# Kernel tuning notes

Hardware: AMD Instinct MI355X
Metric: run time of the kernel (lower is better)

The kernel has to match this reference:

```python
import jax, jax.numpy as jnp
import numpy as np

BS, EMB, RES = 256, 768, 14
N_MASKS, HID, OUT, N_PROJ = 16, 4096, 256, 4
BN_EPS = 1e-5


def setup_inputs() -> dict:
    key = jax.random.key(0)
    ks = jax.random.split(key, 8)
    x = jax.random.normal(ks[0], (BS, EMB, RES, RES), jnp.float32)
    # binary ROI masks over the 14x14 = 196 patch grid
    masks = (jax.random.uniform(ks[1], (BS, N_MASKS, RES * RES)) < 0.3).astype(jnp.float32)
    projection_idx = jax.random.randint(ks[2], (N_MASKS,), 0, N_PROJ, jnp.int32)
    mask_ids = jax.random.randint(ks[3], (BS, N_MASKS), 0, 100, jnp.int32)
    # stacked params for the N_PROJ MLP projectors
    W1 = jax.random.normal(ks[4], (N_PROJ, EMB, HID), jnp.float32) * 0.02
    b1 = jnp.zeros((N_PROJ, HID), jnp.float32)
    gamma = jnp.ones((N_PROJ, HID), jnp.float32)
    beta = jnp.zeros((N_PROJ, HID), jnp.float32)
    W2 = jax.random.normal(ks[5], (N_PROJ, HID, OUT), jnp.float32) * 0.02
    b2 = jnp.zeros((N_PROJ, OUT), jnp.float32)
    return {"x": x, "masks": masks, "projection_idx": projection_idx,
            "mask_ids": mask_ids, "W1": W1, "b1": b1, "gamma": gamma,
            "beta": beta, "W2": W2, "b2": b2}


def reference(x, masks, projection_idx, mask_ids, W1, b1, gamma, beta, W2, b2):
    bs, emb, hx, hy = x.shape
    # [bs, emb, hx, hy] -> [bs, hw, emb]
    emb_local = jnp.transpose(x, (0, 2, 3, 1)).reshape(bs, hx * hy, emb)
    # mask-normalized pooling:  pooled[b,n,:] = mean of embeddings inside mask n
    area = masks.sum(axis=-1, keepdims=True)
    smpl = masks / jnp.maximum(area, 1.0)
    pooled = smpl @ emb_local                       # [bs, n_masks, emb]
    # dense dispatch: run EVERY projector over all pooled tokens (as original)
    h = jnp.einsum('bne,peh->pbnh', pooled, W1) + b1[:, None, None, :]
    # BatchNorm1d in training mode over flattened (bs*n_masks) batch, per projector
    mu = h.mean(axis=(1, 2), keepdims=True)
    var = jnp.mean(jnp.square(h - mu), axis=(1, 2), keepdims=True)  # biased var
    h = (h - mu) * jax.lax.rsqrt(var + BN_EPS) * gamma[:, None, None, :] + beta[:, None, None, :]
    h = jax.nn.relu(h)
    o = jnp.einsum('pbnh,pho->pbno', h, W2) + b2[:, None, None, :]   # [P, bs, n, out]
    # keep only projector projection_idx[n] for mask-slot n (disjoint selection)
    n_proj = W1.shape[0]
    sel = (projection_idx[None, :] == jnp.arange(n_proj)[:, None]).astype(o.dtype)  # [P, n]
    xs = (o * sel[:, None, :, None]).sum(axis=0)     # [bs, n_masks, out]
    return (xs, mask_ids)
```

## Files before the change

### kernel.cpp

```cpp
#include <hip/hip_runtime.h>
#include <hip/hip_bf16.h>

#define BS 256
#define EMB 768
#define HW 196
#define NMASK 16
#define HID 4096
#define OUT 256
#define NPROJ 4
#define MROWS 4096

typedef __attribute__((ext_vector_type(8))) short bf16x8;
typedef __attribute__((ext_vector_type(4))) float f32x4;
typedef __attribute__((ext_vector_type(8))) unsigned short u16x8;

__device__ inline float bf2f(unsigned short u) {
    unsigned int x = ((unsigned int)u) << 16;
    return __builtin_bit_cast(float, x);
}
__device__ inline short f2bfs(float f) {
    return __builtin_bit_cast(short, __float2bfloat16(f));
}

#define GL16(gptr, lptr)                                                     \
    __builtin_amdgcn_global_load_lds(                                        \
        (const __attribute__((address_space(1))) void*)(gptr),               \
        (__attribute__((address_space(3))) void*)(lptr), 16, 0, 0)

__global__ __launch_bounds__(256) void pool_mfma(
    const float* __restrict__ x, const float* __restrict__ masks,
    __hip_bfloat16* __restrict__ pooledG)
{
    __shared__ __align__(16) short afr[7 * 64 * 8];
    __shared__ float inv[NMASK];
    const int ec = blockIdx.x, b = blockIdx.y, tid = threadIdx.x;
    const float* mb = masks + (size_t)b * NMASK * HW;

    for (int s = tid; s < 7 * 64; s += 256) {
        int m = s & 15, kb = ((s >> 4) & 3) * 8 + (s >> 6) * 32;
        short v[8];
        #pragma unroll
        for (int j = 0; j < 8; ++j) {
            int kk = kb + j;
            v[j] = (kk < HW) ? f2bfs(mb[m * HW + kk]) : (short)0;
        }
        #pragma unroll
        for (int j = 0; j < 8; ++j) afr[s * 8 + j] = v[j];
    }
    if (tid >= 192) {
        int l = tid - 192, m = l >> 2, q = l & 3;
        float a = 0.f;
        for (int hw = q; hw < HW; hw += 4) a += mb[m * HW + hw];
        a += __shfl_xor(a, 1);
        a += __shfl_xor(a, 2);
        if (q == 0) inv[m] = 1.0f / fmaxf(a, 1.0f);
    }
    __syncthreads();

    const int lane = tid & 63, w = tid >> 6;
    const int lc = lane & 15, l4 = lane >> 4;
    const int ebase = ec * 192 + w * 48;
    const bf16x8* afv = (const bf16x8*)afr;
    f32x4 acc[3] = {};

    const float* xb0 = x + ((size_t)b * EMB + ebase + lc) * HW;

    for (int kc = 0; kc < 6; ++kc) {
        bf16x8 af = afv[kc * 64 + lane];
        float4 u[3][2];
        #pragma unroll
        for (int t = 0; t < 3; ++t) {
            const float* xr = xb0 + (size_t)(t * 16) * HW + kc * 32 + l4 * 8;
            u[t][0] = *(const float4*)(xr);
            u[t][1] = *(const float4*)(xr + 4);
        }
        #pragma unroll
        for (int t = 0; t < 3; ++t) {
            bf16x8 bf;
            bf[0] = f2bfs(u[t][0].x); bf[1] = f2bfs(u[t][0].y);
            bf[2] = f2bfs(u[t][0].z); bf[3] = f2bfs(u[t][0].w);
            bf[4] = f2bfs(u[t][1].x); bf[5] = f2bfs(u[t][1].y);
            bf[6] = f2bfs(u[t][1].z); bf[7] = f2bfs(u[t][1].w);
            acc[t] = __builtin_amdgcn_mfma_f32_16x16x32_bf16(af, bf, acc[t], 0, 0, 0);
        }
    }
    {
        bf16x8 af = afv[6 * 64 + lane];
        #pragma unroll
        for (int t = 0; t < 3; ++t) {
            bf16x8 bf = {};
            if (l4 == 0) {
                float4 u0 = *(const float4*)(xb0 + (size_t)(t * 16) * HW + 192);
                bf[0] = f2bfs(u0.x); bf[1] = f2bfs(u0.y);
                bf[2] = f2bfs(u0.z); bf[3] = f2bfs(u0.w);
            }
            acc[t] = __builtin_amdgcn_mfma_f32_16x16x32_bf16(af, bf, acc[t], 0, 0, 0);
        }
    }

    #pragma unroll
    for (int t = 0; t < 3; ++t) {
        int e = ebase + t * 16 + lc;
        #pragma unroll
        for (int j = 0; j < 4; ++j) {
            int m = l4 * 4 + j;
            pooledG[((size_t)m * 256 + b) * EMB + e] =
                __float2bfloat16(acc[t][j] * inv[m]);
        }
    }
}

__global__ __launch_bounds__(256) void prep(
    const float* __restrict__ W1, const float* __restrict__ W2,
    const __hip_bfloat16* __restrict__ pg,
    __hip_bfloat16* __restrict__ W1T, __hip_bfloat16* __restrict__ W2T,
    __hip_bfloat16* __restrict__ pgT)
{
    __shared__ __align__(16) char sm[64 * 65 * 4];
    const int bid = blockIdx.x, tid = threadIdx.x;
    if (bid < 4096) {
        const float* src; __hip_bfloat16* dst; int R, C, x, y, z;
        if (bid < 3072) { z = bid / 768; int r = bid % 768; x = r % 64; y = r / 64;
                          src = W1; dst = W1T; R = EMB; C = HID; }
        else            { int b2 = bid - 3072; z = b2 / 256; int r = b2 % 256;
                          x = r % 4; y = r / 4; src = W2; dst = W2T; R = HID; C = OUT; }
        float (*tile)[65] = (float(*)[65])sm;
        const float* s = src + (size_t)z * R * C;
        __hip_bfloat16* d = dst + (size_t)z * R * C;
        const int c0 = x * 64, r0 = y * 64;
        for (int i = tid; i < 4096; i += 256) {
            int r = i >> 6, c = i & 63;
            tile[r][c] = s[(size_t)(r0 + r) * C + c0 + c];
        }
        __syncthreads();
        for (int i = tid; i < 4096; i += 256) {
            int c = i >> 6, r = i & 63;
            d[(size_t)(c0 + c) * R + r0 + r] = __float2bfloat16(tile[r][c]);
        }
    } else {
        const int b3 = bid - 4096;
        const int x = b3 % 12, y = b3 / 12;
        __hip_bfloat16 (*tile)[65] = (__hip_bfloat16(*)[65])sm;
        const int c0 = x * 64, r0 = y * 64;
        for (int i = tid; i < 4096; i += 256) {
            int r = i >> 6, c = i & 63;
            tile[r][c] = pg[(size_t)(r0 + r) * EMB + c0 + c];
        }
        __syncthreads();
        for (int i = tid; i < 4096; i += 256) {
            int c = i >> 6, r = i & 63;
            pgT[(size_t)(c0 + c) * MROWS + r0 + r] = tile[r][c];
        }
    }
}

__global__ __launch_bounds__(256) void meanpool(
    const __hip_bfloat16* __restrict__ PT, float* __restrict__ mp)
{
    const int e = blockIdx.x, tid = threadIdx.x;
    const u16x8* p = (const u16x8*)(PT + (size_t)e * MROWS);
    u16x8 v1 = p[tid], v2 = p[tid + 256];
    float s = 0.f;
    #pragma unroll
    for (int j = 0; j < 8; ++j) s += bf2f((unsigned short)v1[j]) + bf2f((unsigned short)v2[j]);
    #pragma unroll
    for (int o = 1; o < 64; o <<= 1) s += __shfl_xor(s, o);
    __shared__ float wsum[4];
    if ((tid & 63) == 0) wsum[tid >> 6] = s;
    __syncthreads();
    if (tid == 0) mp[e] = (wsum[0] + wsum[1] + wsum[2] + wsum[3]) * (1.0f / 4096.0f);
}

__global__ __launch_bounds__(256) void cgemm(
    const __hip_bfloat16* __restrict__ PT, float* __restrict__ Cpart)
{
    __shared__ __align__(16) __hip_bfloat16 As[128 * 32];
    __shared__ __align__(16) __hip_bfloat16 Bs[128 * 32];
    const int tid = threadIdx.x, lane = tid & 63, wid = tid >> 6;
    const int n0 = blockIdx.x * 128, m0 = blockIdx.y * 128, kbase = blockIdx.z * 512;
    float* Cp = Cpart + (size_t)blockIdx.z * EMB * EMB;
    const int wr = wid >> 1, wc = wid & 1;
    const int l4 = lane >> 4, lc = lane & 15;

    f32x4 acc[4][4] = {};
    for (int k0 = kbase; k0 < kbase + 512; k0 += 32) {
        __syncthreads();
        #pragma unroll
        for (int r = 0; r < 2; ++r) {
            int t = r * 256 + tid;
            int row = t >> 2, ko = (t & 3) * 8;
            GL16(PT + (size_t)(m0 + row) * MROWS + k0 + ko, &As[(r * 256 + wid * 64) * 8]);
        }
        #pragma unroll
        for (int r = 0; r < 2; ++r) {
            int t = r * 256 + tid;
            int row = t >> 2, ko = (t & 3) * 8;
            GL16(PT + (size_t)(n0 + row) * MROWS + k0 + ko, &Bs[(r * 256 + wid * 64) * 8]);
        }
        __syncthreads();
        const bf16x8* Av = (const bf16x8*)As;
        const bf16x8* Bv = (const bf16x8*)Bs;
        bf16x8 a[4], b[4];
        #pragma unroll
        for (int m = 0; m < 4; ++m) a[m] = Av[(wr * 64 + m * 16 + lc) * 4 + l4];
        #pragma unroll
        for (int n = 0; n < 4; ++n) b[n] = Bv[(wc * 64 + n * 16 + lc) * 4 + l4];
        #pragma unroll
        for (int m = 0; m < 4; ++m)
            #pragma unroll
            for (int n = 0; n < 4; ++n)
                acc[m][n] = __builtin_amdgcn_mfma_f32_16x16x32_bf16(a[m], b[n], acc[m][n], 0, 0, 0);
    }
    #pragma unroll
    for (int m = 0; m < 4; ++m)
        #pragma unroll
        for (int n = 0; n < 4; ++n)
            #pragma unroll
            for (int j = 0; j < 4; ++j) {
                int row = m0 + wr * 64 + m * 16 + l4 * 4 + j;
                int col = n0 + wc * 64 + n * 16 + lc;
                Cp[(size_t)row * EMB + col] = acc[m][n][j];
            }
}

__global__ __launch_bounds__(256) void cvt_c(
    const float* __restrict__ Cpart, __hip_bfloat16* __restrict__ Cbf)
{
    int i = (blockIdx.x * 256 + threadIdx.x) * 4;
    float sx = 0.f, sy = 0.f, sz = 0.f, sw = 0.f;
    #pragma unroll
    for (int kz = 0; kz < 8; ++kz) {
        float4 v = *(const float4*)(Cpart + (size_t)kz * EMB * EMB + i);
        sx += v.x; sy += v.y; sz += v.z; sw += v.w;
    }
    const float s = 1.0f / 4096.0f;
    Cbf[i + 0] = __float2bfloat16(sx * s);
    Cbf[i + 1] = __float2bfloat16(sy * s);
    Cbf[i + 2] = __float2bfloat16(sz * s);
    Cbf[i + 3] = __float2bfloat16(sw * s);
}

__global__ __launch_bounds__(256) void ugemm(
    const __hip_bfloat16* __restrict__ W1T, const __hip_bfloat16* __restrict__ Cbf,
    const float* __restrict__ mp,
    float* __restrict__ Eh2p, float* __restrict__ Mup)
{
    __shared__ __align__(16) __hip_bfloat16 As[128 * 32];
    __shared__ __align__(16) __hip_bfloat16 Bs[128 * 32];
    const int tid = threadIdx.x, lane = tid & 63, wid = tid >> 6;
    const int n0 = blockIdx.x * 128, m0 = blockIdx.y * 128, p = blockIdx.z;
    const __hip_bfloat16* Ap = W1T + (size_t)p * HID * EMB;
    const int wr = wid >> 1, wc = wid & 1;
    const int l4 = lane >> 4, lc = lane & 15;

    f32x4 acc[4][4] = {};
    for (int k0 = 0; k0 < EMB; k0 += 32) {
        __syncthreads();
        #pragma unroll
        for (int r = 0; r < 2; ++r) {
            int t = r * 256 + tid;
            int row = t >> 2, ko = (t & 3) * 8;
            GL16(Ap + (size_t)(m0 + row) * EMB + k0 + ko, &As[(r * 256 + wid * 64) * 8]);
        }
        #pragma unroll
        for (int r = 0; r < 2; ++r) {
            int t = r * 256 + tid;
            int row = t >> 2, ko = (t & 3) * 8;
            GL16(Cbf + (size_t)(n0 + row) * EMB + k0 + ko, &Bs[(r * 256 + wid * 64) * 8]);
        }
        __syncthreads();
        const bf16x8* Av = (const bf16x8*)As;
        const bf16x8* Bv = (const bf16x8*)Bs;
        bf16x8 a[4], b[4];
        #pragma unroll
        for (int m = 0; m < 4; ++m) a[m] = Av[(wr * 64 + m * 16 + lc) * 4 + l4];
        #pragma unroll
        for (int n = 0; n < 4; ++n) b[n] = Bv[(wc * 64 + n * 16 + lc) * 4 + l4];
        #pragma unroll
        for (int m = 0; m < 4; ++m)
            #pragma unroll
            for (int n = 0; n < 4; ++n)
                acc[m][n] = __builtin_amdgcn_mfma_f32_16x16x32_bf16(a[m], b[n], acc[m][n], 0, 0, 0);
    }

    float mpv[4];
    #pragma unroll
    for (int n = 0; n < 4; ++n) mpv[n] = mp[n0 + wc * 64 + n * 16 + lc];
    #pragma unroll
    for (int m = 0; m < 4; ++m) {
        #pragma unroll
        for (int j = 0; j < 4; ++j) {
            int row = m0 + wr * 64 + m * 16 + l4 * 4 + j;
            const __hip_bfloat16* wrow = Ap + (size_t)row * EMB;
            float e2 = 0.f, mu = 0.f;
            #pragma unroll
            for (int n = 0; n < 4; ++n) {
                int col = n0 + wc * 64 + n * 16 + lc;
                float wv = bf2f(__builtin_bit_cast(unsigned short, wrow[col]));
                e2 += acc[m][n][j] * wv;
                mu += mpv[n] * wv;
            }
            e2 += __shfl_xor(e2, 1); e2 += __shfl_xor(e2, 2);
            e2 += __shfl_xor(e2, 4); e2 += __shfl_xor(e2, 8);
            mu += __shfl_xor(mu, 1); mu += __shfl_xor(mu, 2);
            mu += __shfl_xor(mu, 4); mu += __shfl_xor(mu, 8);
            if (lc == 0) {
                size_t idx = (((size_t)blockIdx.x * 2 + wc) * NPROJ + p) * HID + row;
                Eh2p[idx] = e2;
                Mup [idx] = mu;
            }
        }
    }
}

__global__ __launch_bounds__(256) void finalize(
    const float* __restrict__ Eh2p, const float* __restrict__ Mup,
    const float* __restrict__ gamma, const float* __restrict__ beta,
    float* __restrict__ sbuf, float* __restrict__ tbuf)
{
    int i = blockIdx.x * 256 + threadIdx.x;
    float e2 = 0.f, mu = 0.f;
    #pragma unroll
    for (int bx = 0; bx < 12; ++bx) {
        e2 += Eh2p[bx * (NPROJ * HID) + i];
        mu += Mup [bx * (NPROJ * HID) + i];
    }
    float var = e2 - mu * mu;
    float is  = rsqrtf(fmaxf(var, 0.0f) + 1e-5f);
    float sc  = gamma[i] * is;
    sbuf[i] = sc;
    tbuf[i] = beta[i] - mu * sc;
}

__global__ __launch_bounds__(512, 2) void gemm1_sel(
    const __hip_bfloat16* __restrict__ A, const __hip_bfloat16* __restrict__ W1T,
    const int* __restrict__ proj,
    const float* __restrict__ sbuf, const float* __restrict__ tbuf,
    __hip_bfloat16* __restrict__ hrelu)
{
    __shared__ __align__(16) short LS[3 * 16384];
    const int tid = threadIdx.x, lane = tid & 63, w = tid >> 6;
    const int wr = w >> 2, wc = w & 3;
    const int lc = lane & 15, l4 = lane >> 4;
    const int n0 = blockIdx.x * 256, m0 = blockIdx.y * 256;
    const int p = proj[blockIdx.y];
    const __hip_bfloat16* Ag = A;
    const __hip_bfloat16* Bg = W1T + (size_t)p * HID * EMB;
    const bf16x8* LSv = (const bf16x8*)LS;

    auto STAGE = [&](int t) {
        const int sb = (t % 3) * 32768;
        #pragma unroll
        for (int ab = 0; ab < 2; ++ab) {
            const __hip_bfloat16* g = ab ? Bg : Ag;
            const int rbase = ab ? n0 : m0;
            #pragma unroll
            for (int i = 0; i < 2; ++i) {
                int c = (w * 2 + i) * 64 + lane;
                int row = c >> 2, ps = c & 3;
                int ls = ps ^ (row & 3);
                const __hip_bfloat16* src =
                    g + (size_t)(rbase + row) * EMB + t * 32 + ls * 8;
                GL16(src, (char*)LS + sb + ab * 16384 + (w * 2 + i) * 1024);
            }
        }
    };

    f32x4 acc[8][4] = {};

    STAGE(0);
    STAGE(1);
    asm volatile("s_waitcnt vmcnt(4)" ::: "memory");
    __builtin_amdgcn_s_barrier();

    for (int t = 0; t < 24; ++t) {
        if (t + 2 < 24) STAGE(t + 2);
        const int vb = (t % 3) * 2048;

        bf16x8 bfr[4];
        #pragma unroll
        for (int nf = 0; nf < 4; ++nf) {
            int rb = wc * 64 + nf * 16 + lc;
            bfr[nf] = LSv[vb + 1024 + rb * 4 + (l4 ^ (rb & 3))];
        }
        #pragma unroll
        for (int q = 0; q < 4; ++q) {
            bf16x8 afr[2];
            #pragma unroll
            for (int m2 = 0; m2 < 2; ++m2) {
                int ra = wr * 128 + (q * 2 + m2) * 16 + lc;
                afr[m2] = LSv[vb + ra * 4 + (l4 ^ (ra & 3))];
            }
            __builtin_amdgcn_s_setprio(1);
            #pragma unroll
            for (int m2 = 0; m2 < 2; ++m2)
                #pragma unroll
                for (int nf = 0; nf < 4; ++nf)
                    acc[q * 2 + m2][nf] = __builtin_amdgcn_mfma_f32_16x16x32_bf16(
                        afr[m2], bfr[nf], acc[q * 2 + m2][nf], 0, 0, 0);
            __builtin_amdgcn_s_setprio(0);
        }

        if (t + 2 < 24) {
            asm volatile("s_waitcnt vmcnt(4)" ::: "memory");
            __builtin_amdgcn_s_barrier();
        } else if (t + 2 == 24) {
            asm volatile("s_waitcnt vmcnt(0)" ::: "memory");
            __builtin_amdgcn_s_barrier();
        }
    }

    #pragma unroll
    for (int nf = 0; nf < 4; ++nf) {
        int col = n0 + wc * 64 + nf * 16 + lc;
        float s = sbuf[p * HID + col];
        float tt = tbuf[p * HID + col];
        #pragma unroll
        for (int mf = 0; mf < 8; ++mf)
            #pragma unroll
            for (int j = 0; j < 4; ++j) {
                int row = m0 + wr * 128 + mf * 16 + l4 * 4 + j;
                float v = fmaxf(acc[mf][nf][j] * s + tt, 0.0f);
                hrelu[(size_t)row * HID + col] = __float2bfloat16(v);
            }
    }
}

__global__ __launch_bounds__(256) void gemm2(
    const __hip_bfloat16* __restrict__ Hn, const __hip_bfloat16* __restrict__ W2T,
    const int* __restrict__ proj, float* __restrict__ Opart)
{
    __shared__ __align__(16) __hip_bfloat16 As[128 * 32];
    __shared__ __align__(16) __hip_bfloat16 Bs[128 * 32];
    const int tid = threadIdx.x, lane = tid & 63, wid = tid >> 6;
    const int nmask = blockIdx.x;
    const int bc    = blockIdx.y;
    const int ct    = blockIdx.z >> 2, kz = blockIdx.z & 3;
    const int p = proj[nmask];
    const __hip_bfloat16* Ap = Hn + (size_t)(nmask * 256 + bc * 128) * HID;
    const __hip_bfloat16* Bp = W2T + ((size_t)p * OUT + ct * 128) * HID;
    float* Op = Opart + (size_t)kz * MROWS * OUT;
    const int wr = wid >> 1, wc = wid & 1;
    const int l4 = lane >> 4, lc = lane & 15;

    f32x4 acc[4][4] = {};
    for (int k0 = kz * 1024; k0 < kz * 1024 + 1024; k0 += 32) {
        __syncthreads();
        #pragma unroll
        for (int r = 0; r < 2; ++r) {
            int t = r * 256 + tid;
            int row = t >> 2, ko = (t & 3) * 8;
            GL16(Ap + (size_t)row * HID + k0 + ko, &As[(r * 256 + wid * 64) * 8]);
        }
        #pragma unroll
        for (int r = 0; r < 2; ++r) {
            int t = r * 256 + tid;
            int row = t >> 2, ko = (t & 3) * 8;
            GL16(Bp + (size_t)row * HID + k0 + ko, &Bs[(r * 256 + wid * 64) * 8]);
        }
        __syncthreads();
        const bf16x8* Av = (const bf16x8*)As;
        const bf16x8* Bv = (const bf16x8*)Bs;
        bf16x8 a[4], b[4];
        #pragma unroll
        for (int m = 0; m < 4; ++m) a[m] = Av[(wr * 64 + m * 16 + lc) * 4 + l4];
        #pragma unroll
        for (int n = 0; n < 4; ++n) b[n] = Bv[(wc * 64 + n * 16 + lc) * 4 + l4];
        #pragma unroll
        for (int m = 0; m < 4; ++m)
            #pragma unroll
            for (int n = 0; n < 4; ++n)
                acc[m][n] = __builtin_amdgcn_mfma_f32_16x16x32_bf16(a[m], b[n], acc[m][n], 0, 0, 0);
    }

    #pragma unroll
    for (int m = 0; m < 4; ++m)
        #pragma unroll
        for (int n = 0; n < 4; ++n)
            #pragma unroll
            for (int j = 0; j < 4; ++j) {
                int bb = bc * 128 + wr * 64 + m * 16 + l4 * 4 + j;
                int oc = ct * 128 + wc * 64 + n * 16 + lc;
                Op[((size_t)bb * NMASK + nmask) * OUT + oc] = acc[m][n][j];
            }
}

__global__ __launch_bounds__(256) void reduce_out(
    const float* __restrict__ Opart, const float* __restrict__ b2,
    const int* __restrict__ proj, const int* __restrict__ mids,
    float* __restrict__ out)
{
    int i = (blockIdx.x * 256 + threadIdx.x) * 4;
    float sx = 0.f, sy = 0.f, sz = 0.f, sw = 0.f;
    #pragma unroll
    for (int kz = 0; kz < 4; ++kz) {
        float4 v = *(const float4*)(Opart + (size_t)kz * MROWS * OUT + i);
        sx += v.x; sy += v.y; sz += v.z; sw += v.w;
    }
    int nm = (i >> 8) & 15;
    int p  = proj[nm];
    float4 bv = *(const float4*)(b2 + p * OUT + (i & 255));
    float4 r;
    r.x = sx + bv.x; r.y = sy + bv.y; r.z = sz + bv.z; r.w = sw + bv.w;
    *(float4*)(out + i) = r;
    if (blockIdx.x < 16) {
        int t = blockIdx.x * 256 + threadIdx.x;
        out[(size_t)MROWS * OUT + t] = (float)mids[t];
    }
}

extern "C" void kernel_launch(void* const* d_in, const int* in_sizes, int n_in,
                              void* d_out, int out_size, void* d_ws, size_t ws_size,
                              hipStream_t stream)
{
    const float* x     = (const float*)d_in[0];
    const float* masks = (const float*)d_in[1];
    const int*   proj  = (const int*)d_in[2];
    const int*   mids  = (const int*)d_in[3];
    const float* W1    = (const float*)d_in[4];
    const float* gamma = (const float*)d_in[6];
    const float* beta  = (const float*)d_in[7];
    const float* W2    = (const float*)d_in[8];
    const float* b2    = (const float*)d_in[9];
    float* out = (float*)d_out;

    char* ws = (char*)d_ws;
    __hip_bfloat16* pooledG = (__hip_bfloat16*)(ws);
    __hip_bfloat16* W1T     = (__hip_bfloat16*)(ws + 6291456);
    __hip_bfloat16* W2T     = (__hip_bfloat16*)(ws + 31457280);
    float*          mp      = (float*)(ws + 39845888);
    float*          Eh2p    = (float*)(ws + 39848960);
    float*          Mup     = (float*)(ws + 40635392);
    float*          sbuf    = (float*)(ws + 41421824);
    float*          tbuf    = (float*)(ws + 41487360);
    char* R = ws + 41552896;
    __hip_bfloat16* pooledT = (__hip_bfloat16*)(R);
    float*          Cpart   = (float*)(R + 6291456);
    __hip_bfloat16* Cbf     = (__hip_bfloat16*)(R + 25165824);
    __hip_bfloat16* hrelu   = (__hip_bfloat16*)(R);
    float*          Opart   = (float*)(R + 33554432);

    pool_mfma<<<dim3(4, BS), 256, 0, stream>>>(x, masks, pooledG);
    prep<<<4864, 256, 0, stream>>>(W1, W2, pooledG, W1T, W2T, pooledT);
    meanpool<<<EMB, 256, 0, stream>>>(pooledT, mp);
    cgemm<<<dim3(6, 6, 8), 256, 0, stream>>>(pooledT, Cpart);
    cvt_c<<<(EMB * EMB) / 1024, 256, 0, stream>>>(Cpart, Cbf);
    ugemm<<<dim3(6, 32, 4), 256, 0, stream>>>(W1T, Cbf, mp, Eh2p, Mup);
    finalize<<<(NPROJ * HID) / 256, 256, 0, stream>>>(Eh2p, Mup, gamma, beta, sbuf, tbuf);
    gemm1_sel<<<dim3(HID / 256, MROWS / 256), 512, 0, stream>>>(pooledG, W1T, proj, sbuf, tbuf, hrelu);
    gemm2<<<dim3(NMASK, 2, 8), 256, 0, stream>>>(hrelu, W2T, proj, Opart);
    reduce_out<<<(MROWS * OUT) / 1024, 256, 0, stream>>>(Opart, b2, proj, mids, out);
}
```

Before: 202.5 us.

## Fuse pooling with weight prep, fold meanpool and BN finalize into neighbors

Merges the pooling kernel with the W1/W2 transpose-convert kernel into one launch, so the two independent jobs can overlap across blocks. The per-embedding mean is now computed as per-batch partial sums inside pooling and reduced in the cvt_c kernel, which replaces the separate meanpool pass over the transposed pooled tensor. The BN finalize kernel is removed and its scale/shift is recomputed per block inside gemm1_sel and kept in shared memory. This cuts the launch count from ten to eight, at the cost of redundant finalize work across row-blocks and a serial 256-step reduction per thread in cvt_c.

```diff
diff --git a/kernel.cpp b/kernel.cpp
--- a/kernel.cpp
+++ b/kernel.cpp
@@ -27,107 +27,109 @@
         (const __attribute__((address_space(1))) void*)(gptr),               \
         (__attribute__((address_space(3))) void*)(lptr), 16, 0, 0)
 
-__global__ __launch_bounds__(256) void pool_mfma(
+__global__ __launch_bounds__(256) void fused_k1(
     const float* __restrict__ x, const float* __restrict__ masks,
-    __hip_bfloat16* __restrict__ pooledG)
-{
-    __shared__ __align__(16) short afr[7 * 64 * 8];
-    __shared__ float inv[NMASK];
-    const int ec = blockIdx.x, b = blockIdx.y, tid = threadIdx.x;
-    const float* mb = masks + (size_t)b * NMASK * HW;
-
-    for (int s = tid; s < 7 * 64; s += 256) {
-        int m = s & 15, kb = ((s >> 4) & 3) * 8 + (s >> 6) * 32;
-        short v[8];
-        #pragma unroll
-        for (int j = 0; j < 8; ++j) {
-            int kk = kb + j;
-            v[j] = (kk < HW) ? f2bfs(mb[m * HW + kk]) : (short)0;
-        }
-        #pragma unroll
-        for (int j = 0; j < 8; ++j) afr[s * 8 + j] = v[j];
-    }
-    if (tid >= 192) {
-        int l = tid - 192, m = l >> 2, q = l & 3;
-        float a = 0.f;
-        for (int hw = q; hw < HW; hw += 4) a += mb[m * HW + hw];
-        a += __shfl_xor(a, 1);
-        a += __shfl_xor(a, 2);
-        if (q == 0) inv[m] = 1.0f / fmaxf(a, 1.0f);
-    }
-    __syncthreads();
-
-    const int lane = tid & 63, w = tid >> 6;
-    const int lc = lane & 15, l4 = lane >> 4;
-    const int ebase = ec * 192 + w * 48;
-    const bf16x8* afv = (const bf16x8*)afr;
-    f32x4 acc[3] = {};
-
-    const float* xb0 = x + ((size_t)b * EMB + ebase + lc) * HW;
-
-    for (int kc = 0; kc < 6; ++kc) {
-        bf16x8 af = afv[kc * 64 + lane];
-        float4 u[3][2];
+    const float* __restrict__ W1, const float* __restrict__ W2,
+    __hip_bfloat16* __restrict__ pooledG,
+    __hip_bfloat16* __restrict__ W1T, __hip_bfloat16* __restrict__ W2T,
+    float* __restrict__ mpB)
+{
+    __shared__ __align__(16) char smu[16704];
+    const int bid = blockIdx.x, tid = threadIdx.x;
+
+    if (bid < 1024) {
+        short* afr = (short*)smu;
+        float* inv = (float*)(smu + 14592);
+        const int ec = bid & 3, b = bid >> 2;
+        const float* mb = masks + (size_t)b * NMASK * HW;
+
+        for (int s = tid; s < 7 * 64; s += 256) {
+            int m = s & 15, kb = ((s >> 4) & 3) * 8 + (s >> 6) * 32;
+            short v[8];
+            #pragma unroll
+            for (int j = 0; j < 8; ++j) {
+                int kk = kb + j;
+                v[j] = (kk < HW) ? f2bfs(mb[m * HW + kk]) : (short)0;
+            }
+            #pragma unroll
+            for (int j = 0; j < 8; ++j) afr[s * 8 + j] = v[j];
+        }
+        if (tid >= 192) {
+            int l = tid - 192, m = l >> 2, q = l & 3;
+            float a = 0.f;
+            for (int hw = q; hw < HW; hw += 4) a += mb[m * HW + hw];
+            a += __shfl_xor(a, 1);
+            a += __shfl_xor(a, 2);
+            if (q == 0) inv[m] = 1.0f / fmaxf(a, 1.0f);
+        }
+        __syncthreads();
+
+        const int lane = tid & 63, w = tid >> 6;
+        const int lc = lane & 15, l4 = lane >> 4;
+        const int ebase = ec * 192 + w * 48;
+        const bf16x8* afv = (const bf16x8*)afr;
+        f32x4 acc[3] = {};
+
+        const float* xb0 = x + ((size_t)b * EMB + ebase + lc) * HW;
+
+        for (int kc = 0; kc < 6; ++kc) {
+            bf16x8 af = afv[kc * 64 + lane];
+            float4 u[3][2];
+            #pragma unroll
+            for (int t = 0; t < 3; ++t) {
+                const float* xr = xb0 + (size_t)(t * 16) * HW + kc * 32 + l4 * 8;
+                u[t][0] = *(const float4*)(xr);
+                u[t][1] = *(const float4*)(xr + 4);
+            }
+            #pragma unroll
+            for (int t = 0; t < 3; ++t) {
+                bf16x8 bf;
+                bf[0] = f2bfs(u[t][0].x); bf[1] = f2bfs(u[t][0].y);
+                bf[2] = f2bfs(u[t][0].z); bf[3] = f2bfs(u[t][0].w);
+                bf[4] = f2bfs(u[t][1].x); bf[5] = f2bfs(u[t][1].y);
+                bf[6] = f2bfs(u[t][1].z); bf[7] = f2bfs(u[t][1].w);
+                acc[t] = __builtin_amdgcn_mfma_f32_16x16x32_bf16(af, bf, acc[t], 0, 0, 0);
+            }
+        }
+        {
+            bf16x8 af = afv[6 * 64 + lane];
+            #pragma unroll
+            for (int t = 0; t < 3; ++t) {
+                bf16x8 bf = {};
+                if (l4 == 0) {
+                    float4 u0 = *(const float4*)(xb0 + (size_t)(t * 16) * HW + 192);
+                    bf[0] = f2bfs(u0.x); bf[1] = f2bfs(u0.y);
+                    bf[2] = f2bfs(u0.z); bf[3] = f2bfs(u0.w);
+                }
+                acc[t] = __builtin_amdgcn_mfma_f32_16x16x32_bf16(af, bf, acc[t], 0, 0, 0);
+            }
+        }
+
         #pragma unroll
         for (int t = 0; t < 3; ++t) {
-            const float* xr = xb0 + (size_t)(t * 16) * HW + kc * 32 + l4 * 8;
-            u[t][0] = *(const float4*)(xr);
-            u[t][1] = *(const float4*)(xr + 4);
-        }
-        #pragma unroll
-        for (int t = 0; t < 3; ++t) {
-            bf16x8 bf;
-            bf[0] = f2bfs(u[t][0].x); bf[1] = f2bfs(u[t][0].y);
-            bf[2] = f2bfs(u[t][0].z); bf[3] = f2bfs(u[t][0].w);
-            bf[4] = f2bfs(u[t][1].x); bf[5] = f2bfs(u[t][1].y);
-            bf[6] = f2bfs(u[t][1].z); bf[7] = f2bfs(u[t][1].w);
-            acc[t] = __builtin_amdgcn_mfma_f32_16x16x32_bf16(af, bf, acc[t], 0, 0, 0);
-        }
-    }
-    {
-        bf16x8 af = afv[6 * 64 + lane];
-        #pragma unroll
-        for (int t = 0; t < 3; ++t) {
-            bf16x8 bf = {};
-            if (l4 == 0) {
-                float4 u0 = *(const float4*)(xb0 + (size_t)(t * 16) * HW + 192);
-                bf[0] = f2bfs(u0.x); bf[1] = f2bfs(u0.y);
-                bf[2] = f2bfs(u0.z); bf[3] = f2bfs(u0.w);
-            }
-            acc[t] = __builtin_amdgcn_mfma_f32_16x16x32_bf16(af, bf, acc[t], 0, 0, 0);
-        }
-    }
-
-    #pragma unroll
-    for (int t = 0; t < 3; ++t) {
-        int e = ebase + t * 16 + lc;
-        #pragma unroll
-        for (int j = 0; j < 4; ++j) {
-            int m = l4 * 4 + j;
-            pooledG[((size_t)m * 256 + b) * EMB + e] =
-                __float2bfloat16(acc[t][j] * inv[m]);
-        }
-    }
-}
-
-__global__ __launch_bounds__(256) void prep(
-    const float* __restrict__ W1, const float* __restrict__ W2,
-    const __hip_bfloat16* __restrict__ pg,
-    __hip_bfloat16* __restrict__ W1T, __hip_bfloat16* __restrict__ W2T,
-    __hip_bfloat16* __restrict__ pgT)
-{
-    __shared__ __align__(16) char sm[64 * 65 * 4];
-    const int bid = blockIdx.x, tid = threadIdx.x;
-    if (bid < 4096) {
-        const float* src; __hip_bfloat16* dst; int R, C, x, y, z;
-        if (bid < 3072) { z = bid / 768; int r = bid % 768; x = r % 64; y = r / 64;
-                          src = W1; dst = W1T; R = EMB; C = HID; }
-        else            { int b2 = bid - 3072; z = b2 / 256; int r = b2 % 256;
-                          x = r % 4; y = r / 4; src = W2; dst = W2T; R = HID; C = OUT; }
-        float (*tile)[65] = (float(*)[65])sm;
+            int e = ebase + t * 16 + lc;
+            float msum = 0.f;
+            #pragma unroll
+            for (int j = 0; j < 4; ++j) {
+                int m = l4 * 4 + j;
+                float v = acc[t][j] * inv[m];
+                msum += v;
+                pooledG[((size_t)m * 256 + b) * EMB + e] = __float2bfloat16(v);
+            }
+            msum += __shfl_xor(msum, 16);
+            msum += __shfl_xor(msum, 32);
+            if (l4 == 0) mpB[(size_t)b * EMB + e] = msum;
+        }
+    } else {
+        const float* src; __hip_bfloat16* dst; int R, C, xx, yy, z;
+        if (bid < 4096) { int idx = bid - 1024; z = idx / 768; int r = idx % 768;
+                          xx = r % 64; yy = r / 64; src = W1; dst = W1T; R = EMB; C = HID; }
+        else            { int idx = bid - 4096; z = idx / 256; int r = idx % 256;
+                          xx = r % 4;  yy = r / 4;  src = W2; dst = W2T; R = HID; C = OUT; }
+        float (*tile)[65] = (float(*)[65])smu;
         const float* s = src + (size_t)z * R * C;
         __hip_bfloat16* d = dst + (size_t)z * R * C;
-        const int c0 = x * 64, r0 = y * 64;
+        const int c0 = xx * 64, r0 = yy * 64;
         for (int i = tid; i < 4096; i += 256) {
             int r = i >> 6, c = i & 63;
             tile[r][c] = s[(size_t)(r0 + r) * C + c0 + c];
@@ -137,38 +139,23 @@
             int c = i >> 6, r = i & 63;
             d[(size_t)(c0 + c) * R + r0 + r] = __float2bfloat16(tile[r][c]);
         }
-    } else {
-        const int b3 = bid - 4096;
-        const int x = b3 % 12, y = b3 / 12;
-        __hip_bfloat16 (*tile)[65] = (__hip_bfloat16(*)[65])sm;
-        const int c0 = x * 64, r0 = y * 64;
-        for (int i = tid; i < 4096; i += 256) {
-            int r = i >> 6, c = i & 63;
-            tile[r][c] = pg[(size_t)(r0 + r) * EMB + c0 + c];
-        }
-        __syncthreads();
-        for (int i = tid; i < 4096; i += 256) {
-            int c = i >> 6, r = i & 63;
-            pgT[(size_t)(c0 + c) * MROWS + r0 + r] = tile[r][c];
-        }
-    }
-}
-
-__global__ __launch_bounds__(256) void meanpool(
-    const __hip_bfloat16* __restrict__ PT, float* __restrict__ mp)
-{
-    const int e = blockIdx.x, tid = threadIdx.x;
-    const u16x8* p = (const u16x8*)(PT + (size_t)e * MROWS);
-    u16x8 v1 = p[tid], v2 = p[tid + 256];
-    float s = 0.f;
-    #pragma unroll
-    for (int j = 0; j < 8; ++j) s += bf2f((unsigned short)v1[j]) + bf2f((unsigned short)v2[j]);
-    #pragma unroll
-    for (int o = 1; o < 64; o <<= 1) s += __shfl_xor(s, o);
-    __shared__ float wsum[4];
-    if ((tid & 63) == 0) wsum[tid >> 6] = s;
+    }
+}
+
+__global__ __launch_bounds__(256) void pgT_kernel(
+    const __hip_bfloat16* __restrict__ src, __hip_bfloat16* __restrict__ dst)
+{
+    __shared__ __hip_bfloat16 tile[64][65];
+    const int c0 = blockIdx.x * 64, r0 = blockIdx.y * 64, tid = threadIdx.x;
+    for (int i = tid; i < 4096; i += 256) {
+        int r = i >> 6, c = i & 63;
+        tile[r][c] = src[(size_t)(r0 + r) * EMB + c0 + c];
+    }
     __syncthreads();
-    if (tid == 0) mp[e] = (wsum[0] + wsum[1] + wsum[2] + wsum[3]) * (1.0f / 4096.0f);
+    for (int i = tid; i < 4096; i += 256) {
+        int c = i >> 6, r = i & 63;
+        dst[(size_t)(c0 + c) * MROWS + r0 + r] = tile[r][c];
+    }
 }
 
 __global__ __launch_bounds__(256) void cgemm(
@@ -224,20 +211,29 @@
 }
 
 __global__ __launch_bounds__(256) void cvt_c(
-    const float* __restrict__ Cpart, __hip_bfloat16* __restrict__ Cbf)
-{
-    int i = (blockIdx.x * 256 + threadIdx.x) * 4;
-    float sx = 0.f, sy = 0.f, sz = 0.f, sw = 0.f;
-    #pragma unroll
-    for (int kz = 0; kz < 8; ++kz) {
-        float4 v = *(const float4*)(Cpart + (size_t)kz * EMB * EMB + i);
-        sx += v.x; sy += v.y; sz += v.z; sw += v.w;
-    }
-    const float s = 1.0f / 4096.0f;
-    Cbf[i + 0] = __float2bfloat16(sx * s);
-    Cbf[i + 1] = __float2bfloat16(sy * s);
-    Cbf[i + 2] = __float2bfloat16(sz * s);
-    Cbf[i + 3] = __float2bfloat16(sw * s);
+    const float* __restrict__ Cpart, const float* __restrict__ mpB,
+    __hip_bfloat16* __restrict__ Cbf, float* __restrict__ mp)
+{
+    const int bid = blockIdx.x, tid = threadIdx.x;
+    if (bid < 576) {
+        int i = (bid * 256 + tid) * 4;
+        float sx = 0.f, sy = 0.f, sz = 0.f, sw = 0.f;
+        #pragma unroll
+        for (int kz = 0; kz < 8; ++kz) {
+            float4 v = *(const float4*)(Cpart + (size_t)kz * EMB * EMB + i);
+            sx += v.x; sy += v.y; sz += v.z; sw += v.w;
+        }
+        const float s = 1.0f / 4096.0f;
+        Cbf[i + 0] = __float2bfloat16(sx * s);
+        Cbf[i + 1] = __float2bfloat16(sy * s);
+        Cbf[i + 2] = __float2bfloat16(sz * s);
+        Cbf[i + 3] = __float2bfloat16(sw * s);
+    } else {
+        int e = (bid - 576) * 256 + tid;
+        float s = 0.f;
+        for (int b = 0; b < 256; ++b) s += mpB[(size_t)b * EMB + e];
+        mp[e] = s * (1.0f / 4096.0f);
+    }
 }
 
 __global__ __launch_bounds__(256) void ugemm(
@@ -313,32 +309,15 @@
     }
 }
 
-__global__ __launch_bounds__(256) void finalize(
-    const float* __restrict__ Eh2p, const float* __restrict__ Mup,
-    const float* __restrict__ gamma, const float* __restrict__ beta,
-    float* __restrict__ sbuf, float* __restrict__ tbuf)
-{
-    int i = blockIdx.x * 256 + threadIdx.x;
-    float e2 = 0.f, mu = 0.f;
-    #pragma unroll
-    for (int bx = 0; bx < 12; ++bx) {
-        e2 += Eh2p[bx * (NPROJ * HID) + i];
-        mu += Mup [bx * (NPROJ * HID) + i];
-    }
-    float var = e2 - mu * mu;
-    float is  = rsqrtf(fmaxf(var, 0.0f) + 1e-5f);
-    float sc  = gamma[i] * is;
-    sbuf[i] = sc;
-    tbuf[i] = beta[i] - mu * sc;
-}
-
 __global__ __launch_bounds__(512, 2) void gemm1_sel(
     const __hip_bfloat16* __restrict__ A, const __hip_bfloat16* __restrict__ W1T,
     const int* __restrict__ proj,
-    const float* __restrict__ sbuf, const float* __restrict__ tbuf,
+    const float* __restrict__ Eh2p, const float* __restrict__ Mup,
+    const float* __restrict__ gamma, const float* __restrict__ beta,
     __hip_bfloat16* __restrict__ hrelu)
 {
     __shared__ __align__(16) short LS[3 * 16384];
+    __shared__ float sS[256], sT[256];
     const int tid = threadIdx.x, lane = tid & 63, w = tid >> 6;
     const int wr = w >> 2, wc = w & 3;
     const int lc = lane & 15, l4 = lane >> 4;
@@ -348,6 +327,21 @@
     const __hip_bfloat16* Bg = W1T + (size_t)p * HID * EMB;
     const bf16x8* LSv = (const bf16x8*)LS;
 
+    if (tid < 256) {
+        int col = n0 + tid;
+        float e2 = 0.f, mu = 0.f;
+        #pragma unroll
+        for (int s = 0; s < 12; ++s) {
+            e2 += Eh2p[((size_t)s * NPROJ + p) * HID + col];
+            mu += Mup [((size_t)s * NPROJ + p) * HID + col];
+        }
+        float var = e2 - mu * mu;
+        float is  = rsqrtf(fmaxf(var, 0.0f) + 1e-5f);
+        float sc  = gamma[p * HID + col] * is;
+        sS[tid] = sc;
+        sT[tid] = beta[p * HID + col] - mu * sc;
+    }
+
     auto STAGE = [&](int t) {
         const int sb = (t % 3) * 32768;
         #pragma unroll
@@ -412,9 +406,10 @@
 
     #pragma unroll
     for (int nf = 0; nf < 4; ++nf) {
-        int col = n0 + wc * 64 + nf * 16 + lc;
-        float s = sbuf[p * HID + col];
-        float tt = tbuf[p * HID + col];
+        int cl = wc * 64 + nf * 16 + lc;
+        int col = n0 + cl;
+        float s = sS[cl];
+        float tt = sT[cl];
         #pragma unroll
         for (int mf = 0; mf < 8; ++mf)
             #pragma unroll
@@ -531,23 +526,20 @@
     float*          mp      = (float*)(ws + 39845888);
     float*          Eh2p    = (float*)(ws + 39848960);
     float*          Mup     = (float*)(ws + 40635392);
-    float*          sbuf    = (float*)(ws + 41421824);
-    float*          tbuf    = (float*)(ws + 41487360);
-    char* R = ws + 41552896;
+    float*          mpB     = (float*)(ws + 41421824);
+    char* R = ws + 42208256;
     __hip_bfloat16* pooledT = (__hip_bfloat16*)(R);
     float*          Cpart   = (float*)(R + 6291456);
     __hip_bfloat16* Cbf     = (__hip_bfloat16*)(R + 25165824);
     __hip_bfloat16* hrelu   = (__hip_bfloat16*)(R);
     float*          Opart   = (float*)(R + 33554432);
 
-    pool_mfma<<<dim3(4, BS), 256, 0, stream>>>(x, masks, pooledG);
-    prep<<<4864, 256, 0, stream>>>(W1, W2, pooledG, W1T, W2T, pooledT);
-    meanpool<<<EMB, 256, 0, stream>>>(pooledT, mp);
+    fused_k1<<<5120, 256, 0, stream>>>(x, masks, W1, W2, pooledG, W1T, W2T, mpB);
+    pgT_kernel<<<dim3(EMB / 64, MROWS / 64), 256, 0, stream>>>(pooledG, pooledT);
     cgemm<<<dim3(6, 6, 8), 256, 0, stream>>>(pooledT, Cpart);
-    cvt_c<<<(EMB * EMB) / 1024, 256, 0, stream>>>(Cpart, Cbf);
+    cvt_c<<<579, 256, 0, stream>>>(Cpart, mpB, Cbf, mp);
     ugemm<<<dim3(6, 32, 4), 256, 0, stream>>>(W1T, Cbf, mp, Eh2p, Mup);
-    finalize<<<(NPROJ * HID) / 256, 256, 0, stream>>>(Eh2p, Mup, gamma, beta, sbuf, tbuf);
-    gemm1_sel<<<dim3(HID / 256, MROWS / 256), 512, 0, stream>>>(pooledG, W1T, proj, sbuf, tbuf, hrelu);
+    gemm1_sel<<<dim3(HID / 256, MROWS / 256), 512, 0, stream>>>(pooledG, W1T, proj, Eh2p, Mup, gamma, beta, hrelu);
     gemm2<<<dim3(NMASK, 2, 8), 256, 0, stream>>>(hrelu, W2T, proj, Opart);
     reduce_out<<<(MROWS * OUT) / 1024, 256, 0, stream>>>(Opart, b2, proj, mids, out);
 }
```

New measurement: 213.6 us. 1.05x slower.

## Split mask fragment prep into separate kernel and widen pooling grid

Applied to the files above, without the earlier changes.

Moves the bf16 conversion of the masks and the inverse-area computation into a new per-batch kernel that writes the MFMA A-fragments and inverse areas to workspace. The pooling kernel now runs 3072 blocks of 64 embedding columns instead of 1024 blocks of 192, issues all x loads up front, and pulls the A-fragments into LDS with global_load_lds. This is meant to raise parallelism and memory-level concurrency on the x read, which dominates this stage, and to stop each block recomputing the mask fragments. The cost is an extra kernel launch and a small workspace round trip.

```diff
diff --git a/kernel.cpp b/kernel.cpp
--- a/kernel.cpp
+++ b/kernel.cpp
@@ -27,25 +27,22 @@
         (const __attribute__((address_space(1))) void*)(gptr),               \
         (__attribute__((address_space(3))) void*)(lptr), 16, 0, 0)
 
-__global__ __launch_bounds__(256) void pool_mfma(
-    const float* __restrict__ x, const float* __restrict__ masks,
-    __hip_bfloat16* __restrict__ pooledG)
-{
-    __shared__ __align__(16) short afr[7 * 64 * 8];
-    __shared__ float inv[NMASK];
-    const int ec = blockIdx.x, b = blockIdx.y, tid = threadIdx.x;
+__global__ __launch_bounds__(256) void maskprep(
+    const float* __restrict__ masks, short* __restrict__ afrG,
+    float* __restrict__ invG)
+{
+    const int b = blockIdx.x, tid = threadIdx.x;
     const float* mb = masks + (size_t)b * NMASK * HW;
-
+    short* ag = afrG + (size_t)b * 3584;
     for (int s = tid; s < 7 * 64; s += 256) {
         int m = s & 15, kb = ((s >> 4) & 3) * 8 + (s >> 6) * 32;
-        short v[8];
+        bf16x8 v;
         #pragma unroll
         for (int j = 0; j < 8; ++j) {
             int kk = kb + j;
             v[j] = (kk < HW) ? f2bfs(mb[m * HW + kk]) : (short)0;
         }
-        #pragma unroll
-        for (int j = 0; j < 8; ++j) afr[s * 8 + j] = v[j];
+        *(bf16x8*)(ag + s * 8) = v;
     }
     if (tid >= 192) {
         int l = tid - 192, m = l >> 2, q = l & 3;
@@ -53,60 +50,72 @@
         for (int hw = q; hw < HW; hw += 4) a += mb[m * HW + hw];
         a += __shfl_xor(a, 1);
         a += __shfl_xor(a, 2);
-        if (q == 0) inv[m] = 1.0f / fmaxf(a, 1.0f);
-    }
+        if (q == 0) invG[b * NMASK + m] = 1.0f / fmaxf(a, 1.0f);
+    }
+}
+
+__global__ __launch_bounds__(256) void pool_main(
+    const float* __restrict__ x, const short* __restrict__ afrG,
+    const float* __restrict__ invG, __hip_bfloat16* __restrict__ pooledG)
+{
+    __shared__ __align__(16) short afr[3584];
+    __shared__ float inv[NMASK];
+    const int bid = blockIdx.x;
+    const int b = bid / 12, ec = bid % 12;
+    const int tid = threadIdx.x, lane = tid & 63, w = tid >> 6;
+    const int lc = lane & 15, l4 = lane >> 4;
+
+    const int e = ec * 64 + w * 16 + lc;
+    const float* xrow = x + ((size_t)b * EMB + e) * HW;
+    float4 u[6][2];
+    #pragma unroll
+    for (int kc = 0; kc < 6; ++kc) {
+        u[kc][0] = *(const float4*)(xrow + kc * 32 + l4 * 8);
+        u[kc][1] = *(const float4*)(xrow + kc * 32 + l4 * 8 + 4);
+    }
+    float4 ut = (l4 == 0) ? *(const float4*)(xrow + 192)
+                          : float4{0.f, 0.f, 0.f, 0.f};
+
+    {
+        const char* src = (const char*)(afrG + (size_t)b * 3584);
+        #pragma unroll
+        for (int r = 0; r < 2; ++r) {
+            int cb = r * 256 + w * 64;
+            if (cb < 448)
+                GL16(src + (size_t)cb * 16 + (size_t)lane * 16,
+                     (char*)afr + cb * 16);
+        }
+    }
+    if (tid < NMASK) inv[tid] = invG[b * NMASK + tid];
     __syncthreads();
 
-    const int lane = tid & 63, w = tid >> 6;
-    const int lc = lane & 15, l4 = lane >> 4;
-    const int ebase = ec * 192 + w * 48;
     const bf16x8* afv = (const bf16x8*)afr;
-    f32x4 acc[3] = {};
-
-    const float* xb0 = x + ((size_t)b * EMB + ebase + lc) * HW;
-
+    f32x4 acc = {};
+    #pragma unroll
     for (int kc = 0; kc < 6; ++kc) {
         bf16x8 af = afv[kc * 64 + lane];
-        float4 u[3][2];
-        #pragma unroll
-        for (int t = 0; t < 3; ++t) {
-            const float* xr = xb0 + (size_t)(t * 16) * HW + kc * 32 + l4 * 8;
-            u[t][0] = *(const float4*)(xr);
-            u[t][1] = *(const float4*)(xr + 4);
-        }
-        #pragma unroll
-        for (int t = 0; t < 3; ++t) {
-            bf16x8 bf;
-            bf[0] = f2bfs(u[t][0].x); bf[1] = f2bfs(u[t][0].y);
-            bf[2] = f2bfs(u[t][0].z); bf[3] = f2bfs(u[t][0].w);
-            bf[4] = f2bfs(u[t][1].x); bf[5] = f2bfs(u[t][1].y);
-            bf[6] = f2bfs(u[t][1].z); bf[7] = f2bfs(u[t][1].w);
-            acc[t] = __builtin_amdgcn_mfma_f32_16x16x32_bf16(af, bf, acc[t], 0, 0, 0);
-        }
+        bf16x8 bf;
+        bf[0] = f2bfs(u[kc][0].x); bf[1] = f2bfs(u[kc][0].y);
+        bf[2] = f2bfs(u[kc][0].z); bf[3] = f2bfs(u[kc][0].w);
+        bf[4] = f2bfs(u[kc][1].x); bf[5] = f2bfs(u[kc][1].y);
+        bf[6] = f2bfs(u[kc][1].z); bf[7] = f2bfs(u[kc][1].w);
+        acc = __builtin_amdgcn_mfma_f32_16x16x32_bf16(af, bf, acc, 0, 0, 0);
     }
     {
         bf16x8 af = afv[6 * 64 + lane];
-        #pragma unroll
-        for (int t = 0; t < 3; ++t) {
-            bf16x8 bf = {};
-            if (l4 == 0) {
-                float4 u0 = *(const float4*)(xb0 + (size_t)(t * 16) * HW + 192);
-                bf[0] = f2bfs(u0.x); bf[1] = f2bfs(u0.y);
-                bf[2] = f2bfs(u0.z); bf[3] = f2bfs(u0.w);
-            }
-            acc[t] = __builtin_amdgcn_mfma_f32_16x16x32_bf16(af, bf, acc[t], 0, 0, 0);
-        }
-    }
-
-    #pragma unroll
-    for (int t = 0; t < 3; ++t) {
-        int e = ebase + t * 16 + lc;
-        #pragma unroll
-        for (int j = 0; j < 4; ++j) {
-            int m = l4 * 4 + j;
-            pooledG[((size_t)m * 256 + b) * EMB + e] =
-                __float2bfloat16(acc[t][j] * inv[m]);
-        }
+        bf16x8 bf = {};
+        if (l4 == 0) {
+            bf[0] = f2bfs(ut.x); bf[1] = f2bfs(ut.y);
+            bf[2] = f2bfs(ut.z); bf[3] = f2bfs(ut.w);
+        }
+        acc = __builtin_amdgcn_mfma_f32_16x16x32_bf16(af, bf, acc, 0, 0, 0);
+    }
+
+    #pragma unroll
+    for (int j = 0; j < 4; ++j) {
+        int m = l4 * 4 + j;
+        pooledG[((size_t)m * 256 + b) * EMB + e] =
+            __float2bfloat16(acc[j] * inv[m]);
     }
 }
 
@@ -533,14 +542,17 @@
     float*          Mup     = (float*)(ws + 40635392);
     float*          sbuf    = (float*)(ws + 41421824);
     float*          tbuf    = (float*)(ws + 41487360);
-    char* R = ws + 41552896;
+    short*          afrG    = (short*)(ws + 41552896);
+    float*          invG    = (float*)(ws + 43387904);
+    char* R = ws + 43404288;
     __hip_bfloat16* pooledT = (__hip_bfloat16*)(R);
     float*          Cpart   = (float*)(R + 6291456);
     __hip_bfloat16* Cbf     = (__hip_bfloat16*)(R + 25165824);
     __hip_bfloat16* hrelu   = (__hip_bfloat16*)(R);
     float*          Opart   = (float*)(R + 33554432);
 
-    pool_mfma<<<dim3(4, BS), 256, 0, stream>>>(x, masks, pooledG);
+    maskprep<<<BS, 256, 0, stream>>>(masks, afrG, invG);
+    pool_main<<<3072, 256, 0, stream>>>(x, afrG, invG, pooledG);
     prep<<<4864, 256, 0, stream>>>(W1, W2, pooledG, W1T, W2T, pooledT);
     meanpool<<<EMB, 256, 0, stream>>>(pooledT, mp);
     cgemm<<<dim3(6, 6, 8), 256, 0, stream>>>(pooledT, Cpart);
```

Result: faster. 194.4 us (median of 2 runs) (-4.0%).
